# Kernel tuning notes

Hardware: AMD Instinct MI355X
Metric: run time of the kernel (lower is better)

The kernel has to match this reference:

```python
import jax, jax.numpy as jnp
import numpy as np

R = 3           # disp_range = (3, 3)
DU = 2 * R + 1  # 7 displacements per axis, 49 total
PNAMES = ['mn_w1','mn_b1','mn_w2','mn_b2','mn_w3','mn_b3','mn_w4','mn_b4','mn_wd','mn_bd','mn_w5','mn_b5','dap_w','dap_b','me_w1','me_b1','me_w2','me_b2','me_w3','me_b3','gz1_w','gz1_b','gr1_w','gr1_b','gq1_w','gq1_b','gz2_w','gz2_b','gr2_w','gr2_b','gq2_w','gq2_b','fh_w1','fh_b1','fh_w2','fh_b2']


def conv2d(x, w, b, stride=(1, 1), padding=((1, 1), (1, 1))):
    y = jax.lax.conv_general_dilated(x, w, stride, padding, dimension_numbers=('NCHW', 'OIHW', 'NCHW'))
    return y + b[None, :, None, None]


def warp_backwards(f, flow):
    # bilinear backward warp with zero padding; flow[:,0]=u (x offset), flow[:,1]=v (y offset)
    B, C, H, W = f.shape
    gy, gx = jnp.meshgrid(jnp.arange(H, dtype=flow.dtype), jnp.arange(W, dtype=flow.dtype), indexing='ij')
    x = gx[None] + flow[:, 0]
    y = gy[None] + flow[:, 1]
    x0, y0 = jnp.floor(x), jnp.floor(y)
    wx, wy = x - x0, y - y0

    def corner(yy, xx, wgt):
        valid = (yy >= 0) & (yy <= H - 1) & (xx >= 0) & (xx <= W - 1)
        yc = jnp.clip(yy, 0, H - 1).astype(jnp.int32)
        xc = jnp.clip(xx, 0, W - 1).astype(jnp.int32)
        g = jax.vmap(lambda fb, yb, xb: fb[:, yb, xb])(f, yc, xc)  # (B,C,H,W)
        return g * (wgt * valid.astype(f.dtype))[:, None]

    return (corner(y0, x0, (1 - wy) * (1 - wx)) + corner(y0, x0 + 1, (1 - wy) * wx)
            + corner(y0 + 1, x0, wy * (1 - wx)) + corner(y0 + 1, x0 + 1, wy * wx))


def gru_step(h, x, wz, bz, wr, br, wq, bq, pad):
    hx = jnp.concatenate([h, x], axis=1)
    z = jax.nn.sigmoid(conv2d(hx, wz, bz, padding=pad))
    r = jax.nn.sigmoid(conv2d(hx, wr, br, padding=pad))
    q = jnp.tanh(conv2d(jnp.concatenate([r * h, x], axis=1), wq, bq, padding=pad))
    return (1.0 - z) * h + z * q


def _run(fmap1, fmap2, h, flow, P):
    B, C, H, W = fmap1.shape
    lrelu, relu = jax.nn.leaky_relu, jax.nn.relu
    # backward warp of fmap2 by current (detached) flow
    f2w = warp_backwards(fmap2, jax.lax.stop_gradient(flow))
    # --- correlation volume: 49 zero-padded shifts of warped fmap2, paired with fmap1 ---
    pad2 = jnp.pad(f2w, ((0, 0), (0, 0), (R, R), (R, R)))
    # k = i*DU + j  <->  shift (di, dj) = (i-R, j-R); shifted[...,y,x] = f2w[y+dj, x+di]
    shifted = jnp.stack([pad2[:, :, j:j + H, i:i + W] for i in range(DU) for j in range(DU)], axis=1)  # (B,49,C,H,W)
    valid = (jnp.sum(shifted, axis=2, keepdims=True) != 0).astype(fmap1.dtype)
    mvol = jnp.concatenate([jnp.broadcast_to(fmap1[:, None], shifted.shape), shifted], axis=2) * valid  # (B,49,2C,H,W)
    # --- matching net, applied per displacement ---
    x = mvol.reshape(B * DU * DU, 2 * C, H, W)
    x = relu(conv2d(x, P['mn_w1'], P['mn_b1']))
    x = relu(conv2d(x, P['mn_w2'], P['mn_b2'], stride=(2, 2)))
    x = relu(conv2d(x, P['mn_w3'], P['mn_b3']))
    x = relu(conv2d(x, P['mn_w4'], P['mn_b4']))
    # ConvTranspose2d(k=4, s=2, p=1) == lhs-dilated conv with pad 2
    x = jax.lax.conv_general_dilated(x, P['mn_wd'], (1, 1), ((2, 2), (2, 2)), lhs_dilation=(2, 2), dimension_numbers=('NCHW', 'OIHW', 'NCHW')) + P['mn_bd'][None, :, None, None]
    x = relu(x)
    x = conv2d(x, P['mn_w5'], P['mn_b5'])  # (B*49, 1, H, W)
    cvol = x.reshape(B, DU * DU, H, W)
    # --- displacement-aware projection: 1x1 conv across the 49 displacement channels ---
    cvol = jnp.einsum('ok,bkhw->bohw', P['dap_w'], cvol) + P['dap_b'][None, :, None, None]
    # --- motion encoder ---
    m = jnp.concatenate([cvol, fmap1, flow], axis=1)  # (B, 49+C+2, H, W)
    m = lrelu(conv2d(m, P['me_w1'], P['me_b1']))
    m = lrelu(conv2d(m, P['me_w2'], P['me_b2']))
    m = conv2d(m, P['me_w3'], P['me_b3'])             # (B, 94, H, W)
    xg = jnp.concatenate([m, flow], axis=1)           # (B, 96, H, W)
    # --- separable conv GRU: horizontal (1x5) then vertical (5x1) pass ---
    h = gru_step(h, xg, P['gz1_w'], P['gz1_b'], P['gr1_w'], P['gr1_b'], P['gq1_w'], P['gq1_b'], ((0, 0), (2, 2)))
    h = gru_step(h, xg, P['gz2_w'], P['gz2_b'], P['gr2_w'], P['gr2_b'], P['gq2_w'], P['gq2_b'], ((2, 2), (0, 0)))
    # --- flow head: softmax over 49 displacements, expectation of displacement grid ---
    s = lrelu(jnp.einsum('oi,bihw->bohw', P['fh_w1'], h) + P['fh_b1'][None, :, None, None])
    s = lrelu(jnp.einsum('oi,bihw->bohw', P['fh_w2'], s) + P['fh_b2'][None, :, None, None])
    prob = jax.nn.softmax(s, axis=1)  # (B, 49, H, W)
    dr = jnp.arange(-R, R + 1, dtype=fmap1.dtype)
    disp = jnp.stack([jnp.broadcast_to(dr[:, None], (DU, DU)), jnp.broadcast_to(dr[None, :], (DU, DU))], axis=0).reshape(2, DU * DU)
    d = jnp.einsum('bkhw,ck->bchw', prob, disp)
    return h, flow + d


def _params(key):
    shapes = {'mn_w1': (96, 64, 3, 3), 'mn_b1': (96,), 'mn_w2': (128, 96, 3, 3), 'mn_b2': (128,), 'mn_w3': (128, 128, 3, 3), 'mn_b3': (128,), 'mn_w4': (64, 128, 3, 3), 'mn_b4': (64,), 'mn_wd': (32, 64, 4, 4), 'mn_bd': (32,), 'mn_w5': (1, 32, 3, 3), 'mn_b5': (1,), 'dap_w': (49, 49), 'dap_b': (49,), 'me_w1': (128, 83, 3, 3), 'me_b1': (128,), 'me_w2': (128, 128, 3, 3), 'me_b2': (128,), 'me_w3': (94, 128, 3, 3), 'me_b3': (94,), 'gz1_w': (128, 224, 1, 5), 'gz1_b': (128,), 'gr1_w': (128, 224, 1, 5), 'gr1_b': (128,), 'gq1_w': (128, 224, 1, 5), 'gq1_b': (128,), 'gz2_w': (128, 224, 5, 1), 'gz2_b': (128,), 'gr2_w': (128, 224, 5, 1), 'gr2_b': (128,), 'gq2_w': (128, 224, 5, 1), 'gq2_b': (128,), 'fh_w1': (256, 128), 'fh_b1': (256,), 'fh_w2': (49, 256), 'fh_b2': (49,)}
    keys = jax.random.split(key, len(shapes))
    return {n: jax.random.normal(k, s, dtype=jnp.float32) * 0.05 for (n, s), k in zip(shapes.items(), keys)}


def setup_inputs():
    key = jax.random.key(0)
    k1, k2, k3, k4, kp = jax.random.split(key, 5)
    B, C, H, W, HID = 2, 32, 64, 96, 128
    inp = {'fmap1': jax.random.normal(k1, (B, C, H, W), jnp.float32),
           'fmap2': jax.random.normal(k2, (B, C, H, W), jnp.float32),
           'h': jax.random.normal(k3, (B, HID, H, W), jnp.float32),
           'flow': jax.random.normal(k4, (B, 2, H, W), jnp.float32),
           'i': 0}
    inp.update(_params(kp))
    return inp


def reference(fmap1, fmap2, h, flow, mn_w1, mn_b1, mn_w2, mn_b2, mn_w3, mn_b3, mn_w4, mn_b4, mn_wd, mn_bd, mn_w5, mn_b5, dap_w, dap_b, me_w1, me_b1, me_w2, me_b2, me_w3, me_b3, gz1_w, gz1_b, gr1_w, gr1_b, gq1_w, gq1_b, gz2_w, gz2_b, gr2_w, gr2_b, gq2_w, gq2_b, fh_w1, fh_b1, fh_w2, fh_b2, i):
    ps = (mn_w1, mn_b1, mn_w2, mn_b2, mn_w3, mn_b3, mn_w4, mn_b4, mn_wd, mn_bd, mn_w5, mn_b5, dap_w, dap_b, me_w1, me_b1, me_w2, me_b2, me_w3, me_b3, gz1_w, gz1_b, gr1_w, gr1_b, gq1_w, gq1_b, gz2_w, gz2_b, gr2_w, gr2_b, gq2_w, gq2_b, fh_w1, fh_b1, fh_w2, fh_b2)
    return _run(fmap1, fmap2, h, flow, dict(zip(PNAMES, ps)))
```

## Files before the change

### kernel.cpp

```cpp
#include <hip/hip_runtime.h>
#include <math.h>

typedef unsigned short u16;
typedef unsigned int u32;
typedef __attribute__((ext_vector_type(8))) short bf16x8;
typedef __attribute__((ext_vector_type(4))) float f32x4;

#define HWW 6144

__device__ __forceinline__ float sigmoidf_(float x) { return 1.f / (1.f + expf(-x)); }
__device__ __forceinline__ float lrelu_(float x) { return x >= 0.f ? x : 0.01f * x; }
__device__ __forceinline__ u16 f2bf(float f) {
    u32 u = __float_as_uint(f);
    u += 0x7fffu + ((u >> 16) & 1u);
    return (u16)(u >> 16);
}
__device__ __forceinline__ float bf2f(u16 h) { return __uint_as_float(((u32)h) << 16); }
__device__ __forceinline__ u32 pk2(float a, float b) { return (u32)f2bf(a) | ((u32)f2bf(b) << 16); }

__device__ __forceinline__ void gload_lds16(const u16* g, u16* l) {
    __builtin_amdgcn_global_load_lds((const __attribute__((address_space(1))) void*)g,
                                     (__attribute__((address_space(3))) void*)l, 16, 0, 0);
}

struct WJob { const float* src; unsigned long dstOff; int OC, rowOff, IC, ICP, NT; unsigned long cum; };
struct WJobs { WJob j[16]; long total; };

__global__ __launch_bounds__(256) void k_wt_all(WJobs J, u16* __restrict__ base)
{
    long i = (long)blockIdx.x * 256 + threadIdx.x;
    if (i >= J.total) return;
    int jb = 0;
    #pragma unroll
    for (int k = 1; k < 16; ++k) if (i >= (long)J.j[k].cum) jb = k;
    WJob w = J.j[jb];
    long local = i - (long)w.cum;
    int c = (int)(local % w.ICP);
    int t = (int)((local / w.ICP) % w.NT);
    int o = (int)(local / ((long)w.ICP * w.NT));
    float val = (c < w.IC) ? w.src[((long)o * w.IC + c) * w.NT + t] : 0.f;
    base[w.dstOff + ((long)(w.rowOff + o) * w.NT + t) * w.ICP + c] = f2bf(val);
}

__global__ __launch_bounds__(256) void k_wt_dq(const float* __restrict__ w, u16* __restrict__ dst)
{
    int i = blockIdx.x * 256 + threadIdx.x;
    if (i >= 32768) return;
    int c = i & 63; int t = (i >> 6) & 3; int o = (i >> 8) & 31; int q = i >> 13;
    int ry = q >> 1, rx = q & 1, ta = t >> 1, tb = t & 1;
    int ky = ry + 2 * ta, kx = rx + 2 * tb;
    float val = w[(((long)o * 64 + c) * 4 + ky) * 4 + kx];
    dst[(long)q * 8192 + o * 256 + t * 64 + c] = f2bf(val);
}

__global__ __launch_bounds__(256) void k_wt5(const float* __restrict__ w, float* __restrict__ wt)
{
    int i = blockIdx.x * 256 + threadIdx.x;
    if (i >= 288) return;
    int t = i % 9, c = i / 9;
    wt[t * 32 + c] = w[c * 9 + t];
}

__global__ void k_catb(const float* __restrict__ a, const float* __restrict__ b, float* __restrict__ d)
{
    int i = threadIdx.x;
    if (i < 128) d[i] = a[i];
    else if (i < 256) d[i] = b[i - 128];
}

__global__ __launch_bounds__(256) void k_prep_f1(const float* __restrict__ fmap1, u16* __restrict__ f1bf)
{
    int gid = blockIdx.x * 256 + threadIdx.x;
    if (gid >= 24576) return;
    int idx = gid >> 1, half = gid & 1;
    int b = idx / HWW, p = idx % HWW;
    const float* fb = fmap1 + (long)b * 32 * HWW + p + (long)(half * 16) * HWW;
    u32 pk[8];
    #pragma unroll
    for (int c2 = 0; c2 < 8; ++c2)
        pk[c2] = pk2(fb[(long)(2 * c2) * HWW], fb[(long)(2 * c2 + 1) * HWW]);
    u16* op = f1bf + ((long)idx << 5) + half * 16;
    ((uint4*)op)[0] = make_uint4(pk[0], pk[1], pk[2], pk[3]);
    ((uint4*)op)[1] = make_uint4(pk[4], pk[5], pk[6], pk[7]);
}

__global__ __launch_bounds__(256) void k_warp(const float* __restrict__ fmap2, const float* __restrict__ flow,
                                              u16* __restrict__ f2wbf, float* __restrict__ cs)
{
    int gid = blockIdx.x * 256 + threadIdx.x;
    if (gid >= 24576) return;
    int idx = gid >> 1, half = gid & 1;
    int b = idx / HWW, p = idx % HWW, y = p / 96, x = p % 96;
    float u = flow[(b * 2 + 0) * HWW + p], v = flow[(b * 2 + 1) * HWW + p];
    float fx = (float)x + u, fy = (float)y + v;
    float fx0 = floorf(fx), fy0 = floorf(fy);
    float wx = fx - fx0, wy = fy - fy0;
    int x0 = (int)fx0, y0i = (int)fy0, x1 = x0 + 1, y1 = y0i + 1;
    bool vx0 = x0 >= 0 && x0 < 96, vx1 = x1 >= 0 && x1 < 96;
    bool vy0 = y0i >= 0 && y0i < 64, vy1 = y1 >= 0 && y1 < 64;
    float m00 = (vy0 && vx0) ? (1.f - wy) * (1.f - wx) : 0.f;
    float m01 = (vy0 && vx1) ? (1.f - wy) * wx : 0.f;
    float m10 = (vy1 && vx0) ? wy * (1.f - wx) : 0.f;
    float m11 = (vy1 && vx1) ? wy * wx : 0.f;
    int cx0 = min(max(x0, 0), 95), cx1 = min(max(x1, 0), 95);
    int cy0 = min(max(y0i, 0), 63), cy1 = min(max(y1, 0), 63);
    int i00 = cy0 * 96 + cx0, i01 = cy0 * 96 + cx1, i10 = cy1 * 96 + cx0, i11 = cy1 * 96 + cx1;
    const float* fb = fmap2 + (long)b * 32 * HWW + (long)(half * 16) * HWW;
    float s = 0.f; u32 pk[8];
    #pragma unroll
    for (int c2 = 0; c2 < 8; ++c2) {
        const float* fa = fb + (long)(2 * c2) * HWW;
        const float* fc = fb + (long)(2 * c2 + 1) * HWW;
        float g0 = m00 * fa[i00] + m01 * fa[i01] + m10 * fa[i10] + m11 * fa[i11];
        float g1 = m00 * fc[i00] + m01 * fc[i01] + m10 * fc[i10] + m11 * fc[i11];
        s += g0 + g1;
        pk[c2] = pk2(g0, g1);
    }
    u16* op = f2wbf + ((long)idx << 5) + half * 16;
    ((uint4*)op)[0] = make_uint4(pk[0], pk[1], pk[2], pk[3]);
    ((uint4*)op)[1] = make_uint4(pk[4], pk[5], pk[6], pk[7]);
    float stot = s + __shfl_xor(s, 1);
    if (half == 0) cs[idx] = stot;
}

template<int BM, int BN, int MODE, int KH, int KW, int PH, int PW, int STRIDE, int ACT, int OUTF32,
         int IH, int IW, int OH, int OW, int ICP, int NKT>
__global__ __launch_bounds__(256) void k_gemm(
    const u16* __restrict__ A0, const u16* __restrict__ A1,
    const float* __restrict__ csm, const u16* __restrict__ Wb,
    const float* __restrict__ bias, const u16* __restrict__ zpg,
    u16* __restrict__ outb, u16* __restrict__ outb2, float* __restrict__ outf,
    int OC, int ldc, int coff, int nOff)
{
    constexpr int WAVES_N = (BN >= 128) ? 2 : 1;
    constexpr int WAVES_M = 4 / WAVES_N;
    constexpr int WTM = BM / WAVES_M;
    constexpr int WTN = BN / WAVES_N;
    constexpr int MF = WTM / 16;
    constexpr int NF = WTN / 16;
    __shared__ u16 As[2][BM * 32];
    __shared__ u16 Bs[2][BN * 32];
    int tid = threadIdx.x, lane = tid & 63, wid = tid >> 6;
    constexpr int AIW = BM / 64;
    constexpr int BG  = BN / 16;
    constexpr int BJW = (BG + 3) / 4;
    int ryz = 0, rxz = 0;
    if (MODE == 2) { ryz = blockIdx.z >> 1; rxz = blockIdx.z & 1; }
    const u16* WbZ = Wb + (MODE == 2 ? (long)blockIdx.z * 32 * 256 : 0);
    int n0 = blockIdx.y * BN;
    int chunk = lane & 3, sub = lane >> 2;

    const u16* aB0[AIW]; const u16* aB1[AIW]; u32 am[AIW];
    #pragma unroll
    for (int j = 0; j < AIW; ++j) {
        int row = wid * (BM / 4) + j * 16 + sub;
        int gm = blockIdx.x * BM + row;
        constexpr int OHW = (MODE == 1) ? 6144 : ((MODE == 2) ? 1536 : OH * OW);
        constexpr int OWW = (MODE == 1) ? 96 : ((MODE == 2) ? 48 : OW);
        int nI = gm / OHW, rem = gm - nI * OHW;
        int y0 = rem / OWW, x0 = rem - y0 * OWW;
        aB1[j] = A0; am[j] = 0;
        if (MODE == 0) {
            aB0[j] = A0 + ((long)nI * IH * IW + (long)y0 * STRIDE * IW + (long)x0 * STRIDE) * ICP + chunk * 8;
            u32 m = 0;
            #pragma unroll
            for (int t = 0; t < KH * KW; ++t) {
                int dy = t / KW - PH, dx = t % KW - PW;
                int iy = y0 * STRIDE + dy, ix = x0 * STRIDE + dx;
                m |= ((iy >= 0 && iy < IH && ix >= 0 && ix < IW) ? 1u : 0u) << t;
            }
            am[j] = m;
        } else if (MODE == 1) {
            int n = nOff + nI, bI = n / 49, kd = n - bI * 49;
            int di = kd / 7 - 3, dj = kd % 7 - 3;
            long bH = (long)bI * 6144;
            aB0[j] = A0 + ((bH + rem) << 5) + chunk * 8;
            aB1[j] = A1 + ((bH + (y0 + dj) * 96 + (x0 + di)) << 5) + chunk * 8;
            u32 m = 0;
            #pragma unroll
            for (int t = 0; t < 9; ++t) {
                int dy = t / 3 - 1, dx = t % 3 - 1;
                int yy = y0 + dy, xx = x0 + dx, ys = yy + dj, xs = xx + di;
                bool v = yy >= 0 && yy < 64 && xx >= 0 && xx < 96 && ys >= 0 && ys < 64 && xs >= 0 && xs < 96;
                if (v) v = (csm[bI * 6144 + ys * 96 + xs] != 0.f);
                m |= (v ? 1u : 0u) << t;
            }
            am[j] = m;
        } else {
            int iy0 = y0 + ryz - 1, ix0 = x0 + rxz - 1;
            aB0[j] = A0 + ((long)nI * 1536 + (long)iy0 * 48 + ix0) * 64 + chunk * 8;
            u32 m = 0;
            #pragma unroll
            for (int t = 0; t < 4; ++t) {
                int ta = t >> 1, tb = t & 1;
                int iy = iy0 + ta, ix = ix0 + tb;
                m |= ((iy >= 0 && iy < 32 && ix >= 0 && ix < 48) ? 1u : 0u) << t;
            }
            am[j] = m;
        }
    }
    const u16* bB[BJW];
    #pragma unroll
    for (int j = 0; j < BJW; ++j) {
        int g = wid + 4 * j;
        int gc = (g < BG) ? g : 0;
        bB[j] = WbZ + (long)(n0 + gc * 16 + sub) * (NKT * 32) + chunk * 8;
    }

    auto stage = [&](int kt, int bn) {
        #pragma unroll
        for (int j = 0; j < AIW; ++j) {
            const u16* g;
            if (MODE == 0) {
                constexpr int KTC = ICP / 32;
                int t = kt / KTC, c0 = (kt - t * KTC) << 5;
                int dy = t / KW - PH, dx = t % KW - PW;
                bool v = (am[j] >> t) & 1u;
                g = v ? aB0[j] + (long)(dy * IW + dx) * ICP + c0 : zpg;
            } else if (MODE == 1) {
                int t = kt >> 1, half = kt & 1;
                int dy = t / 3 - 1, dx = t % 3 - 1;
                bool v = (am[j] >> t) & 1u;
                const u16* b = half ? aB1[j] : aB0[j];
                g = v ? b + ((dy * 96 + dx) << 5) : zpg;
            } else {
                int t = kt >> 1, c0 = (kt & 1) << 5;
                int ta = t >> 1, tb = t & 1;
                bool v = (am[j] >> t) & 1u;
                g = v ? aB0[j] + (ta * 48 + tb) * 64 + c0 : zpg;
            }
            gload_lds16(g, &As[bn][(wid * (BM / 4) + j * 16) * 32]);
        }
        #pragma unroll
        for (int j = 0; j < BJW; ++j) {
            int g = wid + 4 * j;
            if (g < BG) gload_lds16(bB[j] + kt * 32, &Bs[bn][g * 512]);
        }
    };

    int wm = (WAVES_N == 2) ? (wid >> 1) : wid;
    int wn = (WAVES_N == 2) ? (wid & 1) : 0;
    int fr = lane & 15, fg = lane >> 4;
    f32x4 acc[MF][NF];
    #pragma unroll
    for (int i = 0; i < MF; ++i)
        #pragma unroll
        for (int j = 0; j < NF; ++j)
            acc[i][j] = (f32x4){0.f, 0.f, 0.f, 0.f};

    stage(0, 0);
    __syncthreads();

    #pragma unroll
    for (int kt = 0; kt < NKT; ++kt) {
        int cur = kt & 1;
        if (kt + 1 < NKT) stage(kt + 1, cur ^ 1);
        bf16x8 af[MF], bv[NF];
        #pragma unroll
        for (int i = 0; i < MF; ++i)
            af[i] = *(const bf16x8*)&As[cur][(wm * WTM + i * 16 + fr) * 32 + fg * 8];
        #pragma unroll
        for (int j = 0; j < NF; ++j)
            bv[j] = *(const bf16x8*)&Bs[cur][(wn * WTN + j * 16 + fr) * 32 + fg * 8];
        #pragma unroll
        for (int i = 0; i < MF; ++i)
            #pragma unroll
            for (int j = 0; j < NF; ++j)
                acc[i][j] = __builtin_amdgcn_mfma_f32_16x16x32_bf16(af[i], bv[j], acc[i][j], 0, 0, 0);
        if (kt + 1 < NKT) __syncthreads();
    }

    #pragma unroll
    for (int i = 0; i < MF; ++i) {
        #pragma unroll
        for (int j = 0; j < NF; ++j) {
            int nn = n0 + wn * WTN + j * 16 + fr;
            if (nn >= OC) continue;
            #pragma unroll
            for (int rr = 0; rr < 4; ++rr) {
                int mloc = wm * WTM + i * 16 + fg * 4 + rr;
                long gm = (long)blockIdx.x * BM + mloc;
                float v = acc[i][j][rr] + bias[nn];
                if (ACT == 1) v = fmaxf(v, 0.f);
                else if (ACT == 2) v = lrelu_(v);
                if (OUTF32 == 1) {
                    outf[gm * ldc + coff + nn] = v;
                } else if (OUTF32 == 2) {
                    float s = sigmoidf_(v);
                    if (nn < 128) outf[gm * 128 + nn] = s;
                    else outb[gm * 224 + (nn - 128)] = f2bf(s * csm[gm * 128 + (nn - 128)]);
                } else if (OUTF32 == 3 || OUTF32 == 4) {
                    float zv = ((const float*)A1)[gm * 128 + nn];
                    float hnew = (1.f - zv) * csm[gm * 128 + nn] + zv * tanhf(v);
                    if (OUTF32 == 3) {
                        outf[gm * 128 + nn] = hnew;
                        outb[gm * 224 + nn] = f2bf(hnew);
                    } else {
                        int bb = (int)(gm / 6144), pp = (int)(gm - (long)bb * 6144);
                        outf[((long)(bb * 128 + nn)) * 6144 + pp] = hnew;
                        outb[gm * 128 + nn] = f2bf(hnew);
                    }
                } else if (MODE == 2) {
                    int nI = (int)(gm / 1536); int rq = (int)(gm - (long)nI * 1536);
                    int Y = rq / 48, X = rq - (rq / 48) * 48;
                    long di = (((long)nI * 64 + 2 * Y + ryz) * 96 + (2 * X + rxz)) * 32 + nn;
                    outb[di] = f2bf(v);
                } else {
                    long di = gm * ldc + coff + nn;
                    u16 hv = f2bf(v);
                    outb[di] = hv;
                    if (outb2) outb2[di] = hv;
                }
            }
        }
    }
}

__global__ __launch_bounds__(256) void k_conv5n(const u16* __restrict__ x5, const float* __restrict__ w5t,
                                                const float* __restrict__ b5, u16* __restrict__ cvolT,
                                                int N, int n0)
{
    int idx = blockIdx.x * 256 + threadIdx.x;
    if (idx >= N * HWW) return;
    int nl = idx / HWW, p = idx % HWW, y = p / 96, x = p % 96;
    float acc = b5[0];
    #pragma unroll
    for (int t = 0; t < 9; ++t) {
        int iy = y + t / 3 - 1, ix = x + t % 3 - 1;
        if (iy < 0 || iy >= 64 || ix < 0 || ix >= 96) continue;
        const u16* sp = x5 + (((long)nl * HWW + iy * 96 + ix) << 5);
        const float* wt_ = w5t + t * 32;
        #pragma unroll
        for (int c8 = 0; c8 < 4; ++c8) {
            uint4 v = *(const uint4*)(sp + c8 * 8);
            acc = fmaf(bf2f((u16)(v.x & 0xffffu)), wt_[c8 * 8 + 0], acc);
            acc = fmaf(bf2f((u16)(v.x >> 16)),     wt_[c8 * 8 + 1], acc);
            acc = fmaf(bf2f((u16)(v.y & 0xffffu)), wt_[c8 * 8 + 2], acc);
            acc = fmaf(bf2f((u16)(v.y >> 16)),     wt_[c8 * 8 + 3], acc);
            acc = fmaf(bf2f((u16)(v.z & 0xffffu)), wt_[c8 * 8 + 4], acc);
            acc = fmaf(bf2f((u16)(v.z >> 16)),     wt_[c8 * 8 + 5], acc);
            acc = fmaf(bf2f((u16)(v.w & 0xffffu)), wt_[c8 * 8 + 6], acc);
            acc = fmaf(bf2f((u16)(v.w >> 16)),     wt_[c8 * 8 + 7], acc);
        }
    }
    int n = n0 + nl;
    int b = n / 49, k = n - b * 49;
    cvolT[((long)b * HWW + p) * 64 + k] = f2bf(acc);
}

__global__ __launch_bounds__(256) void k_me_tail(const float* __restrict__ fmap1, const float* __restrict__ flow,
                                                 u16* __restrict__ mein)
{
    int gid = blockIdx.x * 256 + threadIdx.x;
    if (gid >= 73728) return;
    int j = gid / 12288, idx = gid - j * 12288;
    int b = idx / HWW, p = idx % HWW;
    int c0 = 49 + j * 8;
    u16* mp = mein + (long)idx * 96;
    #pragma unroll
    for (int q = 0; q < 8; ++q) {
        int c = c0 + q;
        if (c >= 96) break;
        float v;
        if (c < 81) v = fmap1[((long)(b * 32 + (c - 49))) * HWW + p];
        else if (c == 81) v = flow[(b * 2 + 0) * HWW + p];
        else if (c == 82) v = flow[(b * 2 + 1) * HWW + p];
        else v = 0.f;
        mp[c] = f2bf(v);
    }
}

__global__ __launch_bounds__(256) void k_set_head(const float* __restrict__ h, const float* __restrict__ flow,
                                                  float* __restrict__ hst, u16* __restrict__ hx,
                                                  u16* __restrict__ hx2)
{
    int gid = blockIdx.x * 256 + threadIdx.x;
    if (gid >= 49152) return;
    int cq = gid / 12288, idx = gid - cq * 12288;
    int b = idx / HWW, p = idx % HWW;
    int c0 = cq * 32;
    const float* hp = h + (long)b * 128 * HWW + p;
    float* hs = hst + (long)idx * 128;
    u16* hxp = hx + (long)idx * 224;
    #pragma unroll
    for (int c = c0; c < c0 + 32; c += 8) {
        float v[8];
        #pragma unroll
        for (int q = 0; q < 8; ++q) v[q] = hp[(long)(c + q) * HWW];
        *(float4*)&hs[c] = make_float4(v[0], v[1], v[2], v[3]);
        *(float4*)&hs[c + 4] = make_float4(v[4], v[5], v[6], v[7]);
        uint4 pk = make_uint4(pk2(v[0], v[1]), pk2(v[2], v[3]), pk2(v[4], v[5]), pk2(v[6], v[7]));
        *(uint4*)&hxp[c] = pk;
    }
    if (cq == 0) {
        u16 uu = f2bf(flow[(b * 2 + 0) * HWW + p]);
        u16 vv = f2bf(flow[(b * 2 + 1) * HWW + p]);
        long o = (long)idx * 224;
        hx[o + 222] = uu; hx[o + 223] = vv;
        hx2[o + 222] = uu; hx2[o + 223] = vv;
    }
}

__global__ __launch_bounds__(256) void k_soft(const float* __restrict__ s2, const float* __restrict__ flow,
                                              float* __restrict__ outFlow)
{
    int idx = blockIdx.x * 256 + threadIdx.x;
    if (idx >= 12288) return;
    int b = idx / HWW, p = idx % HWW;
    const float* sp = s2 + (long)idx * 64;
    float lg[49];
    #pragma unroll
    for (int k = 0; k < 48; k += 4) {
        float4 v = *(const float4*)&sp[k];
        lg[k] = v.x; lg[k + 1] = v.y; lg[k + 2] = v.z; lg[k + 3] = v.w;
    }
    lg[48] = sp[48];
    float m = -1e30f;
    #pragma unroll
    for (int k = 0; k < 49; ++k) m = fmaxf(m, lg[k]);
    float s = 0.f, a0 = 0.f, a1 = 0.f;
    #pragma unroll
    for (int k = 0; k < 49; ++k) {
        float e = expf(lg[k] - m);
        s += e;
        a0 += e * (float)(k / 7 - 3);
        a1 += e * (float)(k % 7 - 3);
    }
    float inv = 1.f / s;
    outFlow[(long)(b * 2 + 0) * HWW + p] = flow[(long)(b * 2 + 0) * HWW + p] + a0 * inv;
    outFlow[(long)(b * 2 + 1) * HWW + p] = flow[(long)(b * 2 + 1) * HWW + p] + a1 * inv;
}

extern "C" void kernel_launch(void* const* d_in, const int* in_sizes, int n_in,
                              void* d_out, int out_size, void* d_ws, size_t ws_size,
                              hipStream_t stream)
{
    const float* fmap1 = (const float*)d_in[0];
    const float* fmap2 = (const float*)d_in[1];
    const float* h     = (const float*)d_in[2];
    const float* flow  = (const float*)d_in[3];
    int pb = (in_sizes[4] == 1) ? 5 : 4;
    const float* mn_w1 = (const float*)d_in[pb + 0];
    const float* mn_b1 = (const float*)d_in[pb + 1];
    const float* mn_w2 = (const float*)d_in[pb + 2];
    const float* mn_b2 = (const float*)d_in[pb + 3];
    const float* mn_w3 = (const float*)d_in[pb + 4];
    const float* mn_b3 = (const float*)d_in[pb + 5];
    const float* mn_w4 = (const float*)d_in[pb + 6];
    const float* mn_b4 = (const float*)d_in[pb + 7];
    const float* mn_wd = (const float*)d_in[pb + 8];
    const float* mn_bd = (const float*)d_in[pb + 9];
    const float* mn_w5 = (const float*)d_in[pb + 10];
    const float* mn_b5 = (const float*)d_in[pb + 11];
    const float* dap_w = (const float*)d_in[pb + 12];
    const float* dap_b = (const float*)d_in[pb + 13];
    const float* me_w1 = (const float*)d_in[pb + 14];
    const float* me_b1 = (const float*)d_in[pb + 15];
    const float* me_w2 = (const float*)d_in[pb + 16];
    const float* me_b2 = (const float*)d_in[pb + 17];
    const float* me_w3 = (const float*)d_in[pb + 18];
    const float* me_b3 = (const float*)d_in[pb + 19];
    const float* gz1_w = (const float*)d_in[pb + 20];
    const float* gz1_b = (const float*)d_in[pb + 21];
    const float* gr1_w = (const float*)d_in[pb + 22];
    const float* gr1_b = (const float*)d_in[pb + 23];
    const float* gq1_w = (const float*)d_in[pb + 24];
    const float* gq1_b = (const float*)d_in[pb + 25];
    const float* gz2_w = (const float*)d_in[pb + 26];
    const float* gz2_b = (const float*)d_in[pb + 27];
    const float* gr2_w = (const float*)d_in[pb + 28];
    const float* gr2_b = (const float*)d_in[pb + 29];
    const float* gq2_w = (const float*)d_in[pb + 30];
    const float* gq2_b = (const float*)d_in[pb + 31];
    const float* fh_w1 = (const float*)d_in[pb + 32];
    const float* fh_b1 = (const float*)d_in[pb + 33];
    const float* fh_w2 = (const float*)d_in[pb + 34];
    const float* fh_b2 = (const float*)d_in[pb + 35];

    char* wsB = (char*)d_ws;
    size_t off = 0;
    auto alc = [&](size_t bytes) { size_t o = off; off = (off + bytes + 255) & ~(size_t)255; return o; };

    size_t o_zpg  = alc(256);
    size_t o_wc1  = alc(128 * 576 * 2);
    size_t o_wc2  = alc(128 * 864 * 2);
    size_t o_wc3  = alc((size_t)128 * 1152 * 2);
    size_t o_wc4  = alc((size_t)64 * 1152 * 2);
    size_t o_wdq  = alc(32768 * 2);
    size_t o_wme1 = alc(128 * 864 * 2);
    size_t o_wme2 = alc((size_t)128 * 1152 * 2);
    size_t o_wme3 = alc((size_t)128 * 1152 * 2);
    size_t o_wzr1 = alc((size_t)256 * 1120 * 2);
    size_t o_wq1  = alc((size_t)128 * 1120 * 2);
    size_t o_wzr2 = alc((size_t)256 * 1120 * 2);
    size_t o_wq2  = alc((size_t)128 * 1120 * 2);
    size_t o_wfh1 = alc(256 * 128 * 2);
    size_t o_wfh2 = alc(64 * 256 * 2);
    size_t o_wdapb= alc(64 * 64 * 2);
    size_t o_w5t  = alc(288 * 4);
    size_t o_bzr1 = alc(256 * 4);
    size_t o_bzr2 = alc(256 * 4);
    size_t wArenaBytes = off;

    size_t o_f1bf = alc((size_t)12288 * 32 * 2);
    size_t o_f2wb = alc((size_t)12288 * 32 * 2);
    size_t o_cs   = alc(12288 * 4);
    size_t o_cvolT= alc((size_t)12288 * 64 * 2);

    const int CH = 49;
    size_t sharedBase = off;
    size_t offA = sharedBase;
    auto alcA = [&](size_t bytes) { size_t o = offA; offA = (offA + bytes + 255) & ~(size_t)255; return o; };
    size_t o_x1 = alcA((size_t)CH * 6144 * 96 * 2);
    size_t o_x2 = alcA((size_t)98 * 1536 * 128 * 2);
    size_t o_x3 = alcA((size_t)98 * 1536 * 128 * 2);
    size_t o_x4 = alcA((size_t)98 * 1536 * 64 * 2);
    size_t o_x5 = alcA((size_t)98 * 6144 * 32 * 2);
    size_t offB2 = sharedBase;
    auto alcB = [&](size_t bytes) { size_t o = offB2; offB2 = (offB2 + bytes + 255) & ~(size_t)255; return o; };
    size_t o_mein = alcB((size_t)12288 * 96 * 2);
    size_t o_m1   = alcB((size_t)12288 * 128 * 2);
    size_t o_m2   = alcB((size_t)12288 * 128 * 2);
    size_t o_hx   = alcB((size_t)12288 * 224 * 2);
    size_t o_hx2  = alcB((size_t)12288 * 224 * 2);
    size_t o_h2bf = alcB((size_t)12288 * 128 * 2);
    size_t o_s1b  = alcB((size_t)12288 * 256 * 2);
    size_t o_hst  = alcB((size_t)12288 * 128 * 4);
    size_t o_h1f  = alcB((size_t)12288 * 128 * 4);
    size_t o_zf   = alcB((size_t)12288 * 128 * 4);
    size_t o_s2   = alcB((size_t)12288 * 64 * 4);

    u16* wbase = (u16*)wsB;
    u16* zpg  = (u16*)(wsB + o_zpg);
    u16* wdq  = (u16*)(wsB + o_wdq);
    float* w5t = (float*)(wsB + o_w5t);
    float* bzr1 = (float*)(wsB + o_bzr1);
    float* bzr2 = (float*)(wsB + o_bzr2);
    u16* wc1  = (u16*)(wsB + o_wc1);   u16* wc2  = (u16*)(wsB + o_wc2);
    u16* wc3  = (u16*)(wsB + o_wc3);   u16* wc4  = (u16*)(wsB + o_wc4);
    u16* wme1 = (u16*)(wsB + o_wme1);  u16* wme2 = (u16*)(wsB + o_wme2);
    u16* wme3 = (u16*)(wsB + o_wme3);
    u16* wzr1 = (u16*)(wsB + o_wzr1);  u16* wq1  = (u16*)(wsB + o_wq1);
    u16* wzr2 = (u16*)(wsB + o_wzr2);  u16* wq2  = (u16*)(wsB + o_wq2);
    u16* wfh1 = (u16*)(wsB + o_wfh1);  u16* wfh2 = (u16*)(wsB + o_wfh2);
    u16* wdapb= (u16*)(wsB + o_wdapb);

    u16* f1bf = (u16*)(wsB + o_f1bf);  u16* f2wb = (u16*)(wsB + o_f2wb);
    float* cs = (float*)(wsB + o_cs);
    u16* cvolT = (u16*)(wsB + o_cvolT);
    u16* x1 = (u16*)(wsB + o_x1); u16* x2 = (u16*)(wsB + o_x2); u16* x3 = (u16*)(wsB + o_x3);
    u16* x4 = (u16*)(wsB + o_x4); u16* x5 = (u16*)(wsB + o_x5);
    u16* mein = (u16*)(wsB + o_mein);
    u16* m1 = (u16*)(wsB + o_m1); u16* m2 = (u16*)(wsB + o_m2);
    u16* hx = (u16*)(wsB + o_hx); u16* hx2 = (u16*)(wsB + o_hx2);
    u16* h2bf = (u16*)(wsB + o_h2bf);  u16* s1b = (u16*)(wsB + o_s1b);
    float* hst = (float*)(wsB + o_hst); float* h1f = (float*)(wsB + o_h1f);
    float* zf = (float*)(wsB + o_zf);
    float* s2 = (float*)(wsB + o_s2);

    float* outH = (float*)d_out;
    float* outFlow = outH + (long)2 * 128 * HWW;

    auto nb = [](long total, int bs) { return (unsigned)((total + bs - 1) / bs); };

    hipMemsetAsync(wsB, 0, wArenaBytes, stream);
    hipMemsetAsync(wsB + o_cvolT, 0, (size_t)12288 * 64 * 2, stream);

    WJobs J;
    {
        auto mk = [](const float* src, size_t dstOffBytes, int OC, int rowOff, int IC, int ICP, int NT) {
            WJob w; w.src = src; w.dstOff = dstOffBytes / 2; w.OC = OC; w.rowOff = rowOff;
            w.IC = IC; w.ICP = ICP; w.NT = NT; w.cum = 0; return w;
        };
        J.j[0]  = mk(mn_w1, o_wc1, 96, 0, 64, 64, 9);
        J.j[1]  = mk(mn_w2, o_wc2, 128, 0, 96, 96, 9);
        J.j[2]  = mk(mn_w3, o_wc3, 128, 0, 128, 128, 9);
        J.j[3]  = mk(mn_w4, o_wc4, 64, 0, 128, 128, 9);
        J.j[4]  = mk(me_w1, o_wme1, 128, 0, 83, 96, 9);
        J.j[5]  = mk(me_w2, o_wme2, 128, 0, 128, 128, 9);
        J.j[6]  = mk(me_w3, o_wme3, 94, 0, 128, 128, 9);
        J.j[7]  = mk(gz1_w, o_wzr1, 128, 0, 224, 224, 5);
        J.j[8]  = mk(gr1_w, o_wzr1, 128, 128, 224, 224, 5);
        J.j[9]  = mk(gq1_w, o_wq1, 128, 0, 224, 224, 5);
        J.j[10] = mk(gz2_w, o_wzr2, 128, 0, 224, 224, 5);
        J.j[11] = mk(gr2_w, o_wzr2, 128, 128, 224, 224, 5);
        J.j[12] = mk(gq2_w, o_wq2, 128, 0, 224, 224, 5);
        J.j[13] = mk(fh_w1, o_wfh1, 256, 0, 128, 128, 1);
        J.j[14] = mk(fh_w2, o_wfh2, 49, 0, 256, 256, 1);
        J.j[15] = mk(dap_w, o_wdapb, 49, 0, 49, 64, 1);
        long cum = 0;
        for (int k = 0; k < 16; ++k) {
            J.j[k].cum = cum;
            cum += (long)J.j[k].OC * J.j[k].NT * J.j[k].ICP;
        }
        J.total = cum;
    }
    k_wt_all<<<nb(J.total, 256), 256, 0, stream>>>(J, wbase);
    k_wt_dq<<<nb(32768, 256), 256, 0, stream>>>(mn_wd, wdq);
    k_wt5<<<2, 256, 0, stream>>>(mn_w5, w5t);
    k_catb<<<1, 256, 0, stream>>>(gz1_b, gr1_b, bzr1);
    k_catb<<<1, 256, 0, stream>>>(gz2_b, gr2_b, bzr2);

    k_prep_f1<<<nb(24576, 256), 256, 0, stream>>>(fmap1, f1bf);
    k_warp<<<nb(24576, 256), 256, 0, stream>>>(fmap2, flow, f2wb, cs);

    for (int n0 = 0; n0 < 98; n0 += CH) {
        k_gemm<128,96,1,3,3,1,1,1,1,0,64,96,64,96,32,18><<<dim3(2352, 1), 256, 0, stream>>>(
            f1bf, f2wb, cs, wc1, mn_b1, zpg, x1, nullptr, nullptr, 96, 96, 0, n0);
        k_gemm<128,128,0,3,3,1,1,2,1,0,64,96,32,48,96,27><<<dim3(588, 1), 256, 0, stream>>>(
            x1, nullptr, nullptr, wc2, mn_b2, zpg, x2 + (long)n0 * 196608, nullptr, nullptr, 128, 128, 0, 0);
    }
    k_gemm<128,128,0,3,3,1,1,1,1,0,32,48,32,48,128,36><<<dim3(1176, 1), 256, 0, stream>>>(
        x2, nullptr, nullptr, wc3, mn_b3, zpg, x3, nullptr, nullptr, 128, 128, 0, 0);
    k_gemm<128,64,0,3,3,1,1,1,1,0,32,48,32,48,128,36><<<dim3(1176, 1), 256, 0, stream>>>(
        x3, nullptr, nullptr, wc4, mn_b4, zpg, x4, nullptr, nullptr, 64, 64, 0, 0);
    k_gemm<128,32,2,4,4,2,2,1,1,0,32,48,32,48,64,8><<<dim3(1176, 1, 4), 256, 0, stream>>>(
        x4, nullptr, nullptr, wdq, mn_bd, zpg, x5, nullptr, nullptr, 32, 32, 0, 0);
    k_conv5n<<<nb(98L * HWW, 256), 256, 0, stream>>>(x5, w5t, mn_b5, cvolT, 98, 0);

    k_gemm<64,64,0,1,1,0,0,1,0,0,64,96,64,96,64,2><<<dim3(192, 1), 256, 0, stream>>>(
        cvolT, nullptr, nullptr, wdapb, dap_b, zpg, mein, nullptr, nullptr, 49, 96, 0, 0);
    k_me_tail<<<nb(73728, 256), 256, 0, stream>>>(fmap1, flow, mein);

    k_gemm<64,128,0,3,3,1,1,1,2,0,64,96,64,96,96,27><<<dim3(192, 1), 256, 0, stream>>>(
        mein, nullptr, nullptr, wme1, me_b1, zpg, m1, nullptr, nullptr, 128, 128, 0, 0);
    k_gemm<64,128,0,3,3,1,1,1,2,0,64,96,64,96,128,36><<<dim3(192, 1), 256, 0, stream>>>(
        m1, nullptr, nullptr, wme2, me_b2, zpg, m2, nullptr, nullptr, 128, 128, 0, 0);
    k_gemm<64,96,0,3,3,1,1,1,0,0,64,96,64,96,128,36><<<dim3(192, 1), 256, 0, stream>>>(
        m2, nullptr, nullptr, wme3, me_b3, zpg, hx, hx2, nullptr, 94, 224, 128, 0);

    k_set_head<<<nb(49152, 256), 256, 0, stream>>>(h, flow, hst, hx, hx2);
    k_gemm<64,128,0,1,5,0,2,1,0,2,64,96,64,96,224,35><<<dim3(192, 2), 256, 0, stream>>>(
        hx, nullptr, hst, wzr1, bzr1, zpg, hx2, nullptr, zf, 256, 256, 0, 0);
    k_gemm<64,128,0,1,5,0,2,1,0,3,64,96,64,96,224,35><<<dim3(192, 1), 256, 0, stream>>>(
        hx2, (const u16*)zf, hst, wq1, gq1_b, zpg, hx, nullptr, h1f, 128, 128, 0, 0);

    k_gemm<64,128,0,5,1,2,0,1,0,2,64,96,64,96,224,35><<<dim3(192, 2), 256, 0, stream>>>(
        hx, nullptr, h1f, wzr2, bzr2, zpg, hx2, nullptr, zf, 256, 256, 0, 0);
    k_gemm<64,128,0,5,1,2,0,1,0,4,64,96,64,96,224,35><<<dim3(192, 1), 256, 0, stream>>>(
        hx2, (const u16*)zf, h1f, wq2, gq2_b, zpg, h2bf, nullptr, outH, 128, 128, 0, 0);

    k_gemm<64,128,0,1,1,0,0,1,2,0,64,96,64,96,128,4><<<dim3(192, 2), 256, 0, stream>>>(
        h2bf, nullptr, nullptr, wfh1, fh_b1, zpg, s1b, nullptr, nullptr, 256, 256, 0, 0);
    k_gemm<64,64,0,1,1,0,0,1,2,1,64,96,64,96,256,8><<<dim3(192, 1), 256, 0, stream>>>(
        s1b, nullptr, nullptr, wfh2, fh_b2, zpg, nullptr, nullptr, s2, 49, 64, 0, 0);
    k_soft<<<nb(12288, 256), 256, 0, stream>>>(s2, flow, outFlow);
}
```

Baseline: 669.1 us.

## Triple-buffer GEMM LDS staging with explicit vmcnt waits and raw barriers

Moves the implicit-GEMM conv kernel from double to triple buffering in LDS, issuing global→LDS loads two K-tiles ahead. Explicit s_waitcnt vmcnt with a fixed per-stage load count replaces __syncthreads, which allows more loads in flight during the MFMA work. Waves that have no B slice to load issue a dummy load into a scratch LDS buffer so every wave's vmcnt stays uniform. The cost is more LDS per block, which may lower occupancy, plus two barriers per iteration. Correctness now depends on the exact count of loads issued per stage.

```diff
diff --git a/kernel.cpp b/kernel.cpp
--- a/kernel.cpp
+++ b/kernel.cpp
@@ -21,6 +21,19 @@
 __device__ __forceinline__ void gload_lds16(const u16* g, u16* l) {
     __builtin_amdgcn_global_load_lds((const __attribute__((address_space(1))) void*)g,
                                      (__attribute__((address_space(3))) void*)l, 16, 0, 0);
+}
+
+template<int N> __device__ __forceinline__ void waitcnt_vm() {
+    if constexpr (N == 0) asm volatile("s_waitcnt vmcnt(0)" ::: "memory");
+    else if constexpr (N == 2) asm volatile("s_waitcnt vmcnt(2)" ::: "memory");
+    else if constexpr (N == 3) asm volatile("s_waitcnt vmcnt(3)" ::: "memory");
+    else if constexpr (N == 4) asm volatile("s_waitcnt vmcnt(4)" ::: "memory");
+    else asm volatile("s_waitcnt vmcnt(0)" ::: "memory");
+}
+__device__ __forceinline__ void barrier_raw() {
+    asm volatile("" ::: "memory");
+    __builtin_amdgcn_s_barrier();
+    asm volatile("" ::: "memory");
 }
 
 struct WJob { const float* src; unsigned long dstOff; int OC, rowOff, IC, ICP, NT; unsigned long cum; };
@@ -138,12 +151,14 @@
     constexpr int WTN = BN / WAVES_N;
     constexpr int MF = WTM / 16;
     constexpr int NF = WTN / 16;
-    __shared__ u16 As[2][BM * 32];
-    __shared__ u16 Bs[2][BN * 32];
+    __shared__ u16 As[3][BM * 32];
+    __shared__ u16 Bs[3][BN * 32];
+    __shared__ u16 dmy[512];
     int tid = threadIdx.x, lane = tid & 63, wid = tid >> 6;
     constexpr int AIW = BM / 64;
     constexpr int BG  = BN / 16;
     constexpr int BJW = (BG + 3) / 4;
+    constexpr int LPS = AIW + BJW;
     int ryz = 0, rxz = 0;
     if (MODE == 2) { ryz = blockIdx.z >> 1; rxz = blockIdx.z & 1; }
     const u16* WbZ = Wb + (MODE == 2 ? (long)blockIdx.z * 32 * 256 : 0);
@@ -235,6 +250,7 @@
         for (int j = 0; j < BJW; ++j) {
             int g = wid + 4 * j;
             if (g < BG) gload_lds16(bB[j] + kt * 32, &Bs[bn][g * 512]);
+            else gload_lds16(zpg, dmy);
         }
     };
 
@@ -249,12 +265,13 @@
             acc[i][j] = (f32x4){0.f, 0.f, 0.f, 0.f};
 
     stage(0, 0);
-    __syncthreads();
+    if (NKT > 1) stage(1, 1);
+    if (NKT > 1) waitcnt_vm<LPS>(); else waitcnt_vm<0>();
+    barrier_raw();
 
     #pragma unroll
     for (int kt = 0; kt < NKT; ++kt) {
-        int cur = kt & 1;
-        if (kt + 1 < NKT) stage(kt + 1, cur ^ 1);
+        int cur = kt % 3;
         bf16x8 af[MF], bv[NF];
         #pragma unroll
         for (int i = 0; i < MF; ++i)
@@ -267,7 +284,16 @@
             #pragma unroll
             for (int j = 0; j < NF; ++j)
                 acc[i][j] = __builtin_amdgcn_mfma_f32_16x16x32_bf16(af[i], bv[j], acc[i][j], 0, 0, 0);
-        if (kt + 1 < NKT) __syncthreads();
+        if (kt + 1 < NKT) {
+            barrier_raw();
+            if (kt + 2 < NKT) {
+                stage(kt + 2, (kt + 2) % 3);
+                waitcnt_vm<LPS>();
+            } else {
+                waitcnt_vm<0>();
+            }
+            barrier_raw();
+        }
     }
 
     #pragma unroll
```

Result: no change. 659.8 us (-1.4%).
